# Optimization experiments

Measured on AMD Instinct MI355X. Metric: run time of the kernel, lower is better.

## Reference

```python
import jax, jax.numpy as jnp
import numpy as np

N_NODES = 100000
N_EDGES = 1600000
IN_D = 128
OUT_D = 128


def setup_inputs() -> dict:
    key = jax.random.key(0)
    ks = jax.random.split(key, 10)
    scale = 1.0 / np.sqrt(IN_D)
    inp = {
        "x": jax.random.normal(ks[0], (N_NODES, IN_D), dtype=jnp.float32),
        "edge_idx": jax.random.randint(ks[1], (2, N_EDGES), 0, N_NODES, dtype=jnp.int32),
        "W1": jax.random.normal(ks[2], (OUT_D, IN_D), dtype=jnp.float32) * scale,
        "b1": jax.random.normal(ks[3], (OUT_D,), dtype=jnp.float32) * scale,
        "W2": jax.random.normal(ks[4], (OUT_D, IN_D), dtype=jnp.float32) * scale,
        "b2": jax.random.normal(ks[5], (OUT_D,), dtype=jnp.float32) * scale,
        "W3": jax.random.normal(ks[6], (OUT_D, IN_D), dtype=jnp.float32) * scale,
        "b3": jax.random.normal(ks[7], (OUT_D,), dtype=jnp.float32) * scale,
        "W4": jax.random.normal(ks[8], (OUT_D, IN_D), dtype=jnp.float32) * scale,
        "b4": jax.random.normal(ks[9], (OUT_D,), dtype=jnp.float32) * scale,
    }
    return inp


def _message_passing(y, src, dst, num_nodes, add_self=True):
    # original: if add_self: x = x + x  (doubles features)
    if add_self:
        y = y + y
    # gather messages from source nodes, scatter-add into target nodes
    return jax.ops.segment_sum(y[src], dst, num_segments=num_nodes)


def reference(x, edge_idx, W1, b1, W2, b2, W3, b3, W4, b4):
    num_nodes = x.shape[0]
    src, dst = edge_idx[0], edge_idx[1]
    x1 = x @ W1.T + b1
    x2 = _message_passing(x @ W2.T + b2, src, dst, num_nodes)
    x3 = _message_passing(x @ W3.T + b3, src, dst, num_nodes)
    x4 = _message_passing(x @ W4.T + b4, src, dst, num_nodes)
    return jax.nn.sigmoid(x3 + x4) * x2 + x1
```

## Files before the change

### kernel.cpp

```cpp
#include <hip/hip_runtime.h>

__device__ __forceinline__ float bf2f(unsigned short u) {
    union { unsigned int i; float f; } v;
    v.i = ((unsigned int)u) << 16;
    return v.f;
}
__device__ __forceinline__ unsigned short f2bf(float f) {
    union { float f; unsigned int i; } v;
    v.f = f;
    unsigned int x = v.i;
    return (unsigned short)((x + 0x7fffu + ((x >> 16) & 1u)) >> 16);
}

typedef short bf16x8 __attribute__((ext_vector_type(8)));
typedef float f32x4 __attribute__((ext_vector_type(4)));

#define BSHIFT 9
#define BRANGE 512

__global__ void prep_kernel(const float* __restrict__ x,
                            const float* __restrict__ W1, const float* __restrict__ W2,
                            const float* __restrict__ W3, const float* __restrict__ W4,
                            unsigned short* __restrict__ xb, unsigned short* __restrict__ Wb,
                            int* __restrict__ deg, int* __restrict__ bcnt, int M, int nx4)
{
    int i = blockIdx.x * 256 + threadIdx.x;
    if (i < nx4) {
        float4 v = ((const float4*)x)[i];
        unsigned lo = (unsigned)f2bf(v.x) | ((unsigned)f2bf(v.y) << 16);
        unsigned hi = (unsigned)f2bf(v.z) | ((unsigned)f2bf(v.w) << 16);
        uint2 p; p.x = lo; p.y = hi;
        *(uint2*)(xb + (size_t)i * 4) = p;
    }
    if (i < M) deg[i] = 0;
    if (bcnt && i < 256) bcnt[i] = 0;
    if (i < 16384) {
        Wb[i]         = f2bf(W1[i]);
        Wb[16384 + i] = f2bf(W2[i]);
        Wb[32768 + i] = f2bf(W3[i] + W4[i]);
    }
}

__global__ __launch_bounds__(512) void bucket_hist_kernel(
    const int* __restrict__ dst, int* __restrict__ bcnt, int ne, int nb)
{
    __shared__ int h[256];
    int t = threadIdx.x;
    if (t < 256) h[t] = 0;
    __syncthreads();
    for (int i = blockIdx.x * 512 + t; i < ne; i += gridDim.x * 512)
        atomicAdd(&h[dst[i] >> BSHIFT], 1);
    __syncthreads();
    if (t < nb) {
        int c = h[t];
        if (c) atomicAdd(&bcnt[t], c);
    }
}

__global__ __launch_bounds__(256) void bucket_scan_kernel(
    const int* __restrict__ bcnt, int* __restrict__ boff, int* __restrict__ gcur, int nb)
{
    __shared__ int sh[256];
    int t = threadIdx.x;
    int v = (t < nb) ? bcnt[t] : 0;
    sh[t] = v;
    __syncthreads();
    int acc = v;
    for (int off = 1; off < 256; off <<= 1) {
        int y = (t >= off) ? sh[t - off] : 0;
        __syncthreads();
        acc += y;
        sh[t] = acc;
        __syncthreads();
    }
    if (t < nb) {
        boff[t + 1] = acc;
        gcur[t] = acc - v;
    }
    if (t == 0) boff[0] = 0;
}

__global__ __launch_bounds__(512) void bucketize_kernel(
    const int* __restrict__ src, const int* __restrict__ dst,
    int* __restrict__ gcur, int2* __restrict__ bucketed, int ne, int chunk)
{
    __shared__ int cnt[256];
    __shared__ int sbase[256];
    const int t = threadIdx.x;
    const int e0 = blockIdx.x * chunk;
    const int e1 = (e0 + chunk < ne) ? e0 + chunk : ne;

    if (t < 256) cnt[t] = 0;
    __syncthreads();
    for (int e = e0 + t; e < e1; e += 512)
        atomicAdd(&cnt[dst[e] >> BSHIFT], 1);
    __syncthreads();
    if (t < 256) {
        int c = cnt[t];
        sbase[t] = c ? atomicAdd(&gcur[t], c) : 0;
        cnt[t] = 0;
    }
    __syncthreads();
    for (int e = e0 + t; e < e1; e += 512) {
        int d = dst[e];
        int b = d >> BSHIFT;
        int loc = atomicAdd(&cnt[b], 1);
        int2 v; v.x = src[e]; v.y = d;
        bucketed[sbase[b] + loc] = v;
    }
}

__global__ __launch_bounds__(512) void bucket_count_kernel(
    const int2* __restrict__ bucketed, const int* __restrict__ boff,
    int* __restrict__ deg, int M)
{
    __shared__ int cnt[BRANGE];
    const int t = threadIdx.x;
    const int b = blockIdx.x;
    cnt[t] = 0;
    __syncthreads();
    const int lo = boff[b], hi = boff[b + 1];
    for (int i = lo + t; i < hi; i += 512)
        atomicAdd(&cnt[bucketed[i].y & (BRANGE - 1)], 1);
    __syncthreads();
    int node = (b << BSHIFT) + t;
    if (node < M) deg[node] = cnt[t];
}

__global__ __launch_bounds__(512) void bucket_fill_kernel(
    const int2* __restrict__ bucketed, const int* __restrict__ boff,
    const int* __restrict__ offs, int* __restrict__ csr, int M)
{
    __shared__ int cur[BRANGE];
    const int t = threadIdx.x;
    const int b = blockIdx.x;
    int node = (b << BSHIFT) + t;
    cur[t] = (node < M) ? offs[node] : 0;
    __syncthreads();
    const int lo = boff[b], hi = boff[b + 1];
    for (int i = lo + t; i < hi; i += 512) {
        int2 e = bucketed[i];
        int p = atomicAdd(&cur[e.y & (BRANGE - 1)], 1);
        csr[p] = e.x;
    }
}

__global__ void hist_kernel(const int* __restrict__ dst, int* __restrict__ deg, int ne) {
    int e = blockIdx.x * blockDim.x + threadIdx.x;
    if (e < ne) atomicAdd(&deg[dst[e]], 1);
}

__global__ __launch_bounds__(1024) void scan_local_kernel(
    const int* __restrict__ deg, int* __restrict__ offs, int* __restrict__ bsum, int n)
{
    __shared__ int sh[1024];
    int t = threadIdx.x;
    int i = blockIdx.x * 1024 + t;
    int v = (i < n) ? deg[i] : 0;
    sh[t] = v;
    __syncthreads();
    int acc = v;
    for (int off = 1; off < 1024; off <<= 1) {
        int y = (t >= off) ? sh[t - off] : 0;
        __syncthreads();
        acc += y;
        sh[t] = acc;
        __syncthreads();
    }
    if (i < n) offs[i] = acc - v;
    if (t == 1023) bsum[blockIdx.x] = acc;
}

__global__ __launch_bounds__(128) void scan_totals_kernel(
    int* __restrict__ bsum, int* __restrict__ offs, int nb, int n)
{
    __shared__ int sh[128];
    int t = threadIdx.x;
    int v = (t < nb) ? bsum[t] : 0;
    sh[t] = v;
    __syncthreads();
    int acc = v;
    for (int off = 1; off < 128; off <<= 1) {
        int y = (t >= off) ? sh[t - off] : 0;
        __syncthreads();
        acc += y;
        sh[t] = acc;
        __syncthreads();
    }
    if (t < nb) bsum[t] = acc - v;
    if (t == 127) offs[n] = acc;
}

__global__ __launch_bounds__(1024) void scan_finalize_kernel(
    int* __restrict__ offs, const int* __restrict__ bsum, int* __restrict__ cursor, int n)
{
    int i = blockIdx.x * 1024 + threadIdx.x;
    if (i < n) {
        int o = offs[i] + bsum[i >> 10];
        offs[i] = o;
        if (cursor) cursor[i] = o;
    }
}

__global__ __launch_bounds__(256) void fill_csr_ranged_kernel(
    const int* __restrict__ src, const int* __restrict__ dst,
    int* __restrict__ cursor, int* __restrict__ csr, int ne, int rangeSize)
{
    const int r = blockIdx.x & 7;
    const int cb = blockIdx.x >> 3;
    const int nchunk = gridDim.x >> 3;
    const unsigned lo = (unsigned)(r * rangeSize);
    for (int e = cb * 256 + threadIdx.x; e < ne; e += nchunk * 256) {
        int d = dst[e];
        int s = src[e];
        if ((unsigned)(d - lo) < (unsigned)rangeSize) {
            int pos = atomicAdd(&cursor[d], 1);
            csr[pos] = s;
        }
    }
}

template<bool BF16SRC>
__global__ __launch_bounds__(256) void gather_kernel(
    const void* __restrict__ xsrc, const int* __restrict__ offs,
    const int* __restrict__ csr, unsigned short* __restrict__ gb, int M)
{
    const int wave = threadIdx.x >> 6;
    const int lane = threadIdx.x & 63;
    const int node = blockIdx.x * 4 + wave;
    if (node >= M) return;
    const int e0 = offs[node];
    const int e1 = offs[node + 1];

    float s0 = 0.f, s1 = 0.f, t0 = 0.f, t1 = 0.f;
    for (int e = e0; e < e1; e += 8) {
        int id[8];
        float m[8];
#pragma unroll
        for (int j = 0; j < 8; ++j) {
            int ee = e + j;
            bool ok = ee < e1;
            id[j] = csr[ok ? ee : e1 - 1];
            m[j] = ok ? 1.f : 0.f;
        }
#pragma unroll
        for (int j = 0; j < 8; ++j) {
            float lo, hi;
            if (BF16SRC) {
                unsigned v = *(const unsigned*)((const unsigned short*)xsrc +
                                                (size_t)id[j] * 128 + lane * 2);
                lo = bf2f((unsigned short)(v & 0xffffu));
                hi = bf2f((unsigned short)(v >> 16));
            } else {
                float2 v = *(const float2*)((const float*)xsrc +
                                            (size_t)id[j] * 128 + lane * 2);
                lo = v.x;
                hi = v.y;
            }
            if (j & 1) { t0 += m[j] * lo; t1 += m[j] * hi; }
            else       { s0 += m[j] * lo; s1 += m[j] * hi; }
        }
    }
    unsigned pk = (unsigned)f2bf(s0 + t0) | ((unsigned)f2bf(s1 + t1) << 16);
    *(unsigned*)(gb + (size_t)node * 128 + lane * 2) = pk;
}

template<bool XBF16>
__global__ __launch_bounds__(256) void gemm_kernel(
    const void* __restrict__ xsrc, const unsigned short* __restrict__ gb,
    const int* __restrict__ deg, const unsigned short* __restrict__ Wb,
    const float* __restrict__ B1, const float* __restrict__ B2,
    const float* __restrict__ B3, const float* __restrict__ B4,
    float* __restrict__ out, int M)
{
    __shared__ unsigned short x_lds[64 * 136];
    __shared__ unsigned short g_lds[64 * 136];

    const int t = threadIdx.x;
    const int wave = t >> 6;
    const int lane = t & 63;
    const int ln = lane & 15;
    const int quad = lane >> 4;
    const int row0 = blockIdx.x * 64;

    if (XBF16) {
        const unsigned short* xb = (const unsigned short*)xsrc;
#pragma unroll
        for (int i = 0; i < 4; ++i) {
            int c = i * 256 + t;
            int row = c >> 4;
            int koff = (c & 15) * 8;
            int grow = row0 + row;
            if (grow > M - 1) grow = M - 1;
            *(uint4*)&x_lds[row * 136 + koff] =
                *(const uint4*)(xb + (size_t)grow * 128 + koff);
        }
    } else {
        const float* xf = (const float*)xsrc;
#pragma unroll
        for (int i = 0; i < 8; ++i) {
            int c = i * 256 + t;
            int row = c >> 5;
            int koff = (c & 31) * 4;
            int grow = row0 + row;
            if (grow > M - 1) grow = M - 1;
            float4 v = *(const float4*)(xf + (size_t)grow * 128 + koff);
            unsigned p0 = (unsigned)f2bf(v.x) | ((unsigned)f2bf(v.y) << 16);
            unsigned p1 = (unsigned)f2bf(v.z) | ((unsigned)f2bf(v.w) << 16);
            *(unsigned*)&x_lds[row * 136 + koff]     = p0;
            *(unsigned*)&x_lds[row * 136 + koff + 2] = p1;
        }
    }
#pragma unroll
    for (int i = 0; i < 4; ++i) {
        int c = i * 256 + t;
        int row = c >> 4;
        int koff = (c & 15) * 8;
        int grow = row0 + row;
        if (grow > M - 1) grow = M - 1;
        *(uint4*)&g_lds[row * 136 + koff] =
            *(const uint4*)(gb + (size_t)grow * 128 + koff);
    }
    __syncthreads();

    f32x4 acc[3][4][2];
#pragma unroll
    for (int p = 0; p < 3; ++p)
#pragma unroll
        for (int rt = 0; rt < 4; ++rt)
#pragma unroll
            for (int c = 0; c < 2; ++c) {
                acc[p][rt][c][0] = 0.f; acc[p][rt][c][1] = 0.f;
                acc[p][rt][c][2] = 0.f; acc[p][rt][c][3] = 0.f;
            }

#pragma unroll
    for (int kk = 0; kk < 4; ++kk) {
        bf16x8 ax[4], ag[4];
#pragma unroll
        for (int rt = 0; rt < 4; ++rt) {
            ax[rt] = *(const bf16x8*)&x_lds[(rt * 16 + ln) * 136 + kk * 32 + quad * 8];
            ag[rt] = *(const bf16x8*)&g_lds[(rt * 16 + ln) * 136 + kk * 32 + quad * 8];
        }
#pragma unroll
        for (int p = 0; p < 3; ++p) {
#pragma unroll
            for (int c = 0; c < 2; ++c) {
                int col = wave * 32 + c * 16 + ln;
                bf16x8 bw = *(const bf16x8*)(Wb + (size_t)p * 16384 +
                                             (size_t)col * 128 + kk * 32 + quad * 8);
#pragma unroll
                for (int rt = 0; rt < 4; ++rt) {
                    acc[p][rt][c] = __builtin_amdgcn_mfma_f32_16x16x32_bf16(
                        (p == 0) ? ax[rt] : ag[rt], bw, acc[p][rt][c], 0, 0, 0);
                }
            }
        }
    }

#pragma unroll
    for (int rt = 0; rt < 4; ++rt) {
#pragma unroll
        for (int i = 0; i < 4; ++i) {
            int row = row0 + rt * 16 + quad * 4 + i;
            if (row < M) {
                float dg = (float)deg[row];
#pragma unroll
                for (int c = 0; c < 2; ++c) {
                    int col = wave * 32 + c * 16 + ln;
                    float p1 = acc[0][rt][c][i] + B1[col];
                    float h2 = 2.f * (acc[1][rt][c][i] + dg * B2[col]);
                    float z  = 2.f * (acc[2][rt][c][i] + dg * (B3[col] + B4[col]));
                    float g = 1.f / (1.f + __expf(-z));
                    out[(size_t)row * 128 + col] = g * h2 + p1;
                }
            }
        }
    }
}

extern "C" void kernel_launch(void* const* d_in, const int* in_sizes, int n_in,
                              void* d_out, int out_size, void* d_ws, size_t ws_size,
                              hipStream_t stream) {
    const float* x  = (const float*)d_in[0];
    const int* eidx = (const int*)d_in[1];
    const float* W1 = (const float*)d_in[2];
    const float* B1 = (const float*)d_in[3];
    const float* W2 = (const float*)d_in[4];
    const float* B2 = (const float*)d_in[5];
    const float* W3 = (const float*)d_in[6];
    const float* B3 = (const float*)d_in[7];
    const float* W4 = (const float*)d_in[8];
    const float* B4 = (const float*)d_in[9];
    float* out      = (float*)d_out;

    const int M  = in_sizes[0] / 128;
    const int NE = in_sizes[1] / 2;
    const int* src = eidx;
    const int* dst = eidx + NE;

    const int NB = (M + BRANGE - 1) >> BSHIFT;

    auto pad = [](size_t b) { return (b + 127) & ~(size_t)127; };
    const size_t xb_bytes  = pad((size_t)M * 128 * 2);
    const size_t gb_bytes  = pad((size_t)M * 128 * 2);
    const size_t wb_bytes  = pad((size_t)3 * 16384 * 2);
    const size_t deg_bytes = pad((size_t)M * 4);
    const size_t off_bytes = pad((size_t)(M + 1) * 4);
    const size_t csr_bytes = pad((size_t)NE * 4);
    const size_t bkt_bytes = pad((size_t)NE * 8);

    const size_t need_full = xb_bytes + gb_bytes + wb_bytes + deg_bytes + off_bytes +
                             1024 + csr_bytes + bkt_bytes + 4 * 1024;
    const bool full = (NB <= 256) && ws_size >= need_full + 1024;

    char* ws = (char*)d_ws;
    size_t off = 0;
    auto take = [&](size_t bytes) -> char* {
        char* p = ws + off;
        off = (off + bytes + 127) & ~(size_t)127;
        return p;
    };

    const int nbScan = (M + 1023) / 1024;

    if (full) {
        unsigned short* xb = (unsigned short*)take(xb_bytes);
        unsigned short* gb = (unsigned short*)take(gb_bytes);
        unsigned short* Wb = (unsigned short*)take(wb_bytes);
        int* deg   = (int*)take((size_t)M * 4);
        int* offs  = (int*)take((size_t)(M + 1) * 4);
        int* bsum  = (int*)take(256 * 4);
        int* csr   = (int*)take((size_t)NE * 4);
        int2* bkt  = (int2*)take((size_t)NE * 8);
        int* bcnt  = (int*)take(256 * 4);
        int* boff  = (int*)take(257 * 4);
        int* gcur  = (int*)take(256 * 4);

        const int nx4 = M * 128 / 4;
        const int chunk = (NE + 255) / 256;

        prep_kernel<<<(M * 32 + 255) / 256, 256, 0, stream>>>(
            x, W1, W2, W3, W4, xb, Wb, deg, bcnt, M, nx4);
        bucket_hist_kernel<<<256, 512, 0, stream>>>(dst, bcnt, NE, NB);
        bucket_scan_kernel<<<1, 256, 0, stream>>>(bcnt, boff, gcur, NB);
        bucketize_kernel<<<256, 512, 0, stream>>>(src, dst, gcur, bkt, NE, chunk);
        bucket_count_kernel<<<NB, 512, 0, stream>>>(bkt, boff, deg, M);
        scan_local_kernel<<<nbScan, 1024, 0, stream>>>(deg, offs, bsum, M);
        scan_totals_kernel<<<1, 128, 0, stream>>>(bsum, offs, nbScan, M);
        scan_finalize_kernel<<<nbScan, 1024, 0, stream>>>(offs, bsum, nullptr, M);
        bucket_fill_kernel<<<NB, 512, 0, stream>>>(bkt, boff, offs, csr, M);
        gather_kernel<true><<<(M + 3) / 4, 256, 0, stream>>>(xb, offs, csr, gb, M);
        gemm_kernel<true><<<(M + 63) / 64, 256, 0, stream>>>(
            xb, gb, deg, Wb, B1, B2, B3, B4, out, M);
    } else {
        unsigned short* gb = (unsigned short*)take(gb_bytes);
        unsigned short* Wb = (unsigned short*)take(wb_bytes);
        int* deg    = (int*)take((size_t)M * 4);
        int* offs   = (int*)take((size_t)(M + 1) * 4);
        int* cursor = (int*)take((size_t)M * 4);
        int* bsum   = (int*)take(256 * 4);
        int* csr    = (int*)take((size_t)NE * 4);

        const int prep_elems = (M > 16384 ? M : 16384);
        const int rangeSize = (M + 7) / 8;
        prep_kernel<<<(prep_elems + 255) / 256, 256, 0, stream>>>(
            x, W1, W2, W3, W4, gb, Wb, deg, nullptr, M, 0);
        hist_kernel<<<(NE + 255) / 256, 256, 0, stream>>>(dst, deg, NE);
        scan_local_kernel<<<nbScan, 1024, 0, stream>>>(deg, offs, bsum, M);
        scan_totals_kernel<<<1, 128, 0, stream>>>(bsum, offs, nbScan, M);
        scan_finalize_kernel<<<nbScan, 1024, 0, stream>>>(offs, bsum, cursor, M);
        fill_csr_ranged_kernel<<<2048, 256, 0, stream>>>(src, dst, cursor, csr, NE, rangeSize);
        gather_kernel<false><<<(M + 3) / 4, 256, 0, stream>>>(x, offs, csr, gb, M);
        gemm_kernel<false><<<(M + 63) / 64, 256, 0, stream>>>(
            x, gb, deg, Wb, B1, B2, B3, B4, out, M);
    }
}
```

Before: 288.2 us.

## Fuse neighbor gather into GEMM kernel, keeping aggregated features in LDS

```diff
diff --git a/kernel.cpp b/kernel.cpp
--- a/kernel.cpp
+++ b/kernel.cpp
@@ -220,61 +220,17 @@
     }
 }
 
-template<bool BF16SRC>
-__global__ __launch_bounds__(256) void gather_kernel(
+template<bool XBF16>
+__global__ __launch_bounds__(256) void fused_gather_gemm_kernel(
     const void* __restrict__ xsrc, const int* __restrict__ offs,
-    const int* __restrict__ csr, unsigned short* __restrict__ gb, int M)
-{
-    const int wave = threadIdx.x >> 6;
-    const int lane = threadIdx.x & 63;
-    const int node = blockIdx.x * 4 + wave;
-    if (node >= M) return;
-    const int e0 = offs[node];
-    const int e1 = offs[node + 1];
-
-    float s0 = 0.f, s1 = 0.f, t0 = 0.f, t1 = 0.f;
-    for (int e = e0; e < e1; e += 8) {
-        int id[8];
-        float m[8];
-#pragma unroll
-        for (int j = 0; j < 8; ++j) {
-            int ee = e + j;
-            bool ok = ee < e1;
-            id[j] = csr[ok ? ee : e1 - 1];
-            m[j] = ok ? 1.f : 0.f;
-        }
-#pragma unroll
-        for (int j = 0; j < 8; ++j) {
-            float lo, hi;
-            if (BF16SRC) {
-                unsigned v = *(const unsigned*)((const unsigned short*)xsrc +
-                                                (size_t)id[j] * 128 + lane * 2);
-                lo = bf2f((unsigned short)(v & 0xffffu));
-                hi = bf2f((unsigned short)(v >> 16));
-            } else {
-                float2 v = *(const float2*)((const float*)xsrc +
-                                            (size_t)id[j] * 128 + lane * 2);
-                lo = v.x;
-                hi = v.y;
-            }
-            if (j & 1) { t0 += m[j] * lo; t1 += m[j] * hi; }
-            else       { s0 += m[j] * lo; s1 += m[j] * hi; }
-        }
-    }
-    unsigned pk = (unsigned)f2bf(s0 + t0) | ((unsigned)f2bf(s1 + t1) << 16);
-    *(unsigned*)(gb + (size_t)node * 128 + lane * 2) = pk;
-}
-
-template<bool XBF16>
-__global__ __launch_bounds__(256) void gemm_kernel(
-    const void* __restrict__ xsrc, const unsigned short* __restrict__ gb,
-    const int* __restrict__ deg, const unsigned short* __restrict__ Wb,
+    const int* __restrict__ csr, const unsigned short* __restrict__ Wb,
     const float* __restrict__ B1, const float* __restrict__ B2,
     const float* __restrict__ B3, const float* __restrict__ B4,
     float* __restrict__ out, int M)
 {
     __shared__ unsigned short x_lds[64 * 136];
     __shared__ unsigned short g_lds[64 * 136];
+    __shared__ float sdeg[64];
 
     const int t = threadIdx.x;
     const int wave = t >> 6;
@@ -311,15 +267,46 @@
             *(unsigned*)&x_lds[row * 136 + koff + 2] = p1;
         }
     }
-#pragma unroll
-    for (int i = 0; i < 4; ++i) {
-        int c = i * 256 + t;
-        int row = c >> 4;
-        int koff = (c & 15) * 8;
-        int grow = row0 + row;
-        if (grow > M - 1) grow = M - 1;
-        *(uint4*)&g_lds[row * 136 + koff] =
-            *(const uint4*)(gb + (size_t)grow * 128 + koff);
+
+    for (int r = 0; r < 16; ++r) {
+        const int row = wave * 16 + r;
+        int node = row0 + row;
+        if (node > M - 1) node = M - 1;
+        const int e0 = offs[node];
+        const int e1 = offs[node + 1];
+
+        float s0 = 0.f, s1 = 0.f, t0 = 0.f, t1 = 0.f;
+        for (int e = e0; e < e1; e += 8) {
+            int id[8];
+            float m[8];
+#pragma unroll
+            for (int j = 0; j < 8; ++j) {
+                int ee = e + j;
+                bool ok = ee < e1;
+                id[j] = csr[ok ? ee : e1 - 1];
+                m[j] = ok ? 1.f : 0.f;
+            }
+#pragma unroll
+            for (int j = 0; j < 8; ++j) {
+                float lo, hi;
+                if (XBF16) {
+                    unsigned v = *(const unsigned*)((const unsigned short*)xsrc +
+                                                    (size_t)id[j] * 128 + lane * 2);
+                    lo = bf2f((unsigned short)(v & 0xffffu));
+                    hi = bf2f((unsigned short)(v >> 16));
+                } else {
+                    float2 v = *(const float2*)((const float*)xsrc +
+                                                (size_t)id[j] * 128 + lane * 2);
+                    lo = v.x;
+                    hi = v.y;
+                }
+                if (j & 1) { t0 += m[j] * lo; t1 += m[j] * hi; }
+                else       { s0 += m[j] * lo; s1 += m[j] * hi; }
+            }
+        }
+        unsigned pk = (unsigned)f2bf(s0 + t0) | ((unsigned)f2bf(s1 + t1) << 16);
+        *(unsigned*)&g_lds[row * 136 + lane * 2] = pk;
+        if (lane == 0) sdeg[row] = (float)(e1 - e0);
     }
     __syncthreads();
 
@@ -362,9 +349,10 @@
     for (int rt = 0; rt < 4; ++rt) {
 #pragma unroll
         for (int i = 0; i < 4; ++i) {
-            int row = row0 + rt * 16 + quad * 4 + i;
+            int lrow = rt * 16 + quad * 4 + i;
+            int row = row0 + lrow;
             if (row < M) {
-                float dg = (float)deg[row];
+                float dg = sdeg[lrow];
 #pragma unroll
                 for (int c = 0; c < 2; ++c) {
                     int col = wave * 32 + c * 16 + ln;
@@ -403,14 +391,13 @@
 
     auto pad = [](size_t b) { return (b + 127) & ~(size_t)127; };
     const size_t xb_bytes  = pad((size_t)M * 128 * 2);
-    const size_t gb_bytes  = pad((size_t)M * 128 * 2);
     const size_t wb_bytes  = pad((size_t)3 * 16384 * 2);
     const size_t deg_bytes = pad((size_t)M * 4);
     const size_t off_bytes = pad((size_t)(M + 1) * 4);
     const size_t csr_bytes = pad((size_t)NE * 4);
     const size_t bkt_bytes = pad((size_t)NE * 8);
 
-    const size_t need_full = xb_bytes + gb_bytes + wb_bytes + deg_bytes + off_bytes +
+    const size_t need_full = xb_bytes + wb_bytes + deg_bytes + off_bytes +
                              1024 + csr_bytes + bkt_bytes + 4 * 1024;
     const bool full = (NB <= 256) && ws_size >= need_full + 1024;
 
@@ -426,7 +413,6 @@
 
     if (full) {
         unsigned short* xb = (unsigned short*)take(xb_bytes);
-        unsigned short* gb = (unsigned short*)take(gb_bytes);
         unsigned short* Wb = (unsigned short*)take(wb_bytes);
         int* deg   = (int*)take((size_t)M * 4);
         int* offs  = (int*)take((size_t)(M + 1) * 4);
@@ -450,29 +436,27 @@
         scan_totals_kernel<<<1, 128, 0, stream>>>(bsum, offs, nbScan, M);
         scan_finalize_kernel<<<nbScan, 1024, 0, stream>>>(offs, bsum, nullptr, M);
         bucket_fill_kernel<<<NB, 512, 0, stream>>>(bkt, boff, offs, csr, M);
-        gather_kernel<true><<<(M + 3) / 4, 256, 0, stream>>>(xb, offs, csr, gb, M);
-        gemm_kernel<true><<<(M + 63) / 64, 256, 0, stream>>>(
-            xb, gb, deg, Wb, B1, B2, B3, B4, out, M);
+        fused_gather_gemm_kernel<true><<<(M + 63) / 64, 256, 0, stream>>>(
+            xb, offs, csr, Wb, B1, B2, B3, B4, out, M);
     } else {
-        unsigned short* gb = (unsigned short*)take(gb_bytes);
         unsigned short* Wb = (unsigned short*)take(wb_bytes);
         int* deg    = (int*)take((size_t)M * 4);
         int* offs   = (int*)take((size_t)(M + 1) * 4);
         int* cursor = (int*)take((size_t)M * 4);
         int* bsum   = (int*)take(256 * 4);
         int* csr    = (int*)take((size_t)NE * 4);
+        unsigned short* xb_unused = nullptr; (void)xb_unused;
 
         const int prep_elems = (M > 16384 ? M : 16384);
         const int rangeSize = (M + 7) / 8;
         prep_kernel<<<(prep_elems + 255) / 256, 256, 0, stream>>>(
-            x, W1, W2, W3, W4, gb, Wb, deg, nullptr, M, 0);
+            x, W1, W2, W3, W4, nullptr, Wb, deg, nullptr, M, 0);
         hist_kernel<<<(NE + 255) / 256, 256, 0, stream>>>(dst, deg, NE);
         scan_local_kernel<<<nbScan, 1024, 0, stream>>>(deg, offs, bsum, M);
         scan_totals_kernel<<<1, 128, 0, stream>>>(bsum, offs, nbScan, M);
         scan_finalize_kernel<<<nbScan, 1024, 0, stream>>>(offs, bsum, cursor, M);
         fill_csr_ranged_kernel<<<2048, 256, 0, stream>>>(src, dst, cursor, csr, NE, rangeSize);
-        gather_kernel<false><<<(M + 3) / 4, 256, 0, stream>>>(x, offs, csr, gb, M);
-        gemm_kernel<false><<<(M + 63) / 64, 256, 0, stream>>>(
-            x, gb, deg, Wb, B1, B2, B3, B4, out, M);
-    }
-}
+        fused_gather_gemm_kernel<false><<<(M + 63) / 64, 256, 0, stream>>>(
+            x, offs, csr, Wb, B1, B2, B3, B4, out, M);
+    }
+}
```

Result: slower. 369.7 us (+28.3%).
